# Performance work log

Measured on AMD Instinct MI355X. Metric: run time of the kernel, lower is better.

Reference implementation:

```python
import jax, jax.numpy as jnp
import numpy as np

B, TP, TF = 256, 128, 64
COV, D, OUT, CTRL, H, L = 64, 64, 32, 128, 512, 2


def _gru_layer(x, Wih, Whh, bih, bhh):
    # x: [B, T, in]; torch GRU gate order: r, z, n
    xg = jnp.einsum('bti,gi->btg', x, Wih) + bih  # [B, T, 3H]
    h0 = jnp.zeros((x.shape[0], Whh.shape[1]), x.dtype)

    def step(h, xg_t):
        gh = h @ Whh.T + bhh
        xr, xz, xn = jnp.split(xg_t, 3, axis=-1)
        hr, hz, hn = jnp.split(gh, 3, axis=-1)
        r = jax.nn.sigmoid(xr + hr)
        z = jax.nn.sigmoid(xz + hz)
        n = jnp.tanh(xn + r * hn)
        h = (1.0 - z) * n + z * h
        return h, h

    _, hs = jax.lax.scan(step, h0, jnp.swapaxes(xg, 0, 1))
    return jnp.swapaxes(hs, 0, 1)  # [B, T, H]


def setup_inputs() -> dict:
    key = jax.random.key(0)
    ks = jax.random.split(key, 32)
    s = 0.05
    inp = {
        'past_input': jax.random.normal(ks[0], (B, TP, COV), jnp.float32),
        'past_label': jax.random.normal(ks[1], (B, TP, OUT), jnp.float32),
        'future_input': jax.random.normal(ks[2], (B, TF, COV), jnp.float32),
        'gru_Wih_0': s * jax.random.normal(ks[3], (3 * H, COV), jnp.float32),
        'gru_Whh_0': s * jax.random.normal(ks[4], (3 * H, H), jnp.float32),
        'gru_bih_0': s * jax.random.normal(ks[5], (3 * H,), jnp.float32),
        'gru_bhh_0': s * jax.random.normal(ks[6], (3 * H,), jnp.float32),
        'gru_Wih_1': s * jax.random.normal(ks[7], (3 * H, H), jnp.float32),
        'gru_Whh_1': s * jax.random.normal(ks[8], (3 * H, H), jnp.float32),
        'gru_bih_1': s * jax.random.normal(ks[9], (3 * H,), jnp.float32),
        'gru_bhh_1': s * jax.random.normal(ks[10], (3 * H,), jnp.float32),
        'flow_u': s * jax.random.normal(ks[11], (D,), jnp.float32),
        'flow_w': s * jax.random.normal(ks[12], (D,), jnp.float32),
        'flow_b': s * jax.random.normal(ks[13], (D,), jnp.float32),
        'feat_W': s * jax.random.normal(ks[14], (D, H), jnp.float32),
        'feat_b': s * jax.random.normal(ks[15], (D,), jnp.float32),
        'ctrl_W1': s * jax.random.normal(ks[16], (CTRL, OUT), jnp.float32),
        'ctrl_b1': s * jax.random.normal(ks[17], (CTRL,), jnp.float32),
        'ctrl_W2': s * jax.random.normal(ks[18], (2 * D, CTRL), jnp.float32),
        'ctrl_b2': s * jax.random.normal(ks[19], (2 * D,), jnp.float32),
        'ctrlmu_W': s * jax.random.normal(ks[20], (D, D), jnp.float32),
        'ctrlmu_b': s * jax.random.normal(ks[21], (D,), jnp.float32),
        'out_W': s * jax.random.normal(ks[22], (OUT, D), jnp.float32),
        'out_b': s * jax.random.normal(ks[23], (OUT,), jnp.float32),
    }
    return inp


def reference(past_input, past_label, future_input,
              gru_Wih_0, gru_Whh_0, gru_bih_0, gru_bhh_0,
              gru_Wih_1, gru_Whh_1, gru_bih_1, gru_bhh_1,
              flow_u, flow_w, flow_b, feat_W, feat_b,
              ctrl_W1, ctrl_b1, ctrl_W2, ctrl_b2,
              ctrlmu_W, ctrlmu_b, out_W, out_b):
    cov = jnp.concatenate([past_input, future_input], axis=1)  # [B, T, COV]
    h1 = _gru_layer(cov, gru_Wih_0, gru_Whh_0, gru_bih_0, gru_bhh_0)
    cov_feat = _gru_layer(h1, gru_Wih_1, gru_Whh_1, gru_bih_1, gru_bhh_1)  # [B, T, H]
    Tp = past_input.shape[1]
    bsz = past_input.shape[0]

    def trans(mu_past, var_past, cov_t):
        # per-dim PlanarFlow vectorized over transition_dim
        a = jnp.tanh(flow_w * mu_past + flow_b)
        mu_prior = flow_u * a + cov_t @ feat_W.T + feat_b + mu_past
        coef = flow_u * flow_w * (1.0 - a * a)
        var_prior = 2.0 * coef * var_past + var_past + 1.0
        return mu_prior, var_prior

    def control(ctrl_in, mu_prior):
        hdn = jnp.tanh(ctrl_in @ ctrl_W1.T + ctrl_b1)
        cm, cls = jnp.split(hdn @ ctrl_W2.T + ctrl_b2, 2, axis=-1)
        cm = cm - (mu_prior @ ctrlmu_W.T + ctrlmu_b)
        return cm, jax.nn.softplus(cls)

    def fuse(mu_pr, var_pr, mu_po, var_po):
        s = var_po + var_pr
        mu_w = (var_po / s) * mu_pr + (var_pr / s) * mu_po
        return mu_w, var_pr * var_po / s

    def past_step(carry, xs):
        mu_post, var_post = carry
        cov_t, lab_t = xs
        mu_pr, var_pr = trans(mu_post, var_post, cov_t)
        pred = mu_pr @ out_W.T + out_b
        cm, cs = control(lab_t, mu_pr)
        return fuse(mu_pr, var_pr, cm, cs), (pred, cm, cs)

    def fut_step(carry, cov_t):
        mu_post, var_post = carry
        mu_pr, var_pr = trans(mu_post, var_post, cov_t)
        pred = mu_pr @ out_W.T + out_b
        cm, cs = control(pred, mu_pr)
        return fuse(mu_pr, var_pr, cm, cs), (pred, cm, cs)

    init = (jnp.zeros((bsz, D), cov.dtype), jnp.ones((bsz, D), cov.dtype))
    cov_p = jnp.swapaxes(cov_feat[:, :Tp], 0, 1)
    lab_p = jnp.swapaxes(past_label, 0, 1)
    carry, (pp, cmp_, csp) = jax.lax.scan(past_step, init, (cov_p, lab_p))
    cov_f = jnp.swapaxes(cov_feat[:, Tp:], 0, 1)
    _, (pf, cmf, csf) = jax.lax.scan(fut_step, carry, cov_f)

    pred = jnp.swapaxes(jnp.concatenate([pp, pf], axis=0), 0, 1)        # [B, T, OUT]
    cm = jnp.swapaxes(jnp.concatenate([cmp_, cmf], axis=0), 0, 1)[:, 1:]  # [B, T-1, D]
    cs = jnp.swapaxes(jnp.concatenate([csp, csf], axis=0), 0, 1)[:, 1:]   # [B, T-1, D]
    return pred, cm, cs
```

## Files before the change

kernel.cpp:

```cpp
#include <hip/hip_runtime.h>
#include <stdint.h>

#define DEV static __device__ __forceinline__

using short8 = __attribute__((ext_vector_type(8))) short;
using f32x4  = __attribute__((ext_vector_type(4))) float;
using gbl_u32 = const __attribute__((address_space(1))) unsigned int;
using lds_u32 = __attribute__((address_space(3))) unsigned int;

DEV float bf2f(short s) {
  unsigned u = ((unsigned)(unsigned short)s) << 16;
  float f; __builtin_memcpy(&f, &u, 4); return f;
}
DEV short f2bf(float f) {
  unsigned u; __builtin_memcpy(&u, &f, 4);
  u = (u + 0x7fffu + ((u >> 16) & 1u)) >> 16;
  return (short)u;
}
DEV void gload_lds16(const void* g, void* l) {
  __builtin_amdgcn_global_load_lds((gbl_u32*)g, (lds_u32*)l, 16, 0, 0);
}
DEV float sigm(float x) { return 1.f / (1.f + __expf(-x)); }
DEV float tanh_f(float x) {
  float e = __expf(2.f * x);
  return 1.f - 2.f * __builtin_amdgcn_rcpf(e + 1.f);
}
DEV unsigned load_sc0(const unsigned int* p) {
  unsigned v;
  asm volatile("global_load_dword %0, %1, off sc0\n\ts_waitcnt vmcnt(0)"
               : "=v"(v) : "v"(p) : "memory");
  return v;
}
DEV unsigned load_agent(const unsigned int* p) {
  return __hip_atomic_load(p, __ATOMIC_RELAXED, __HIP_MEMORY_SCOPE_AGENT);
}
DEV void bar() {
  asm volatile("s_waitcnt lgkmcnt(0)" ::: "memory");
  __builtin_amdgcn_sched_barrier(0);
  __builtin_amdgcn_s_barrier();
  __builtin_amdgcn_sched_barrier(0);
}

__global__ void pack_covf_k(const float* __restrict__ past, const float* __restrict__ fut,
                            short* __restrict__ covf) {
  const int n = 192 * 16 * 2 * 512;
  for (int i = blockIdx.x * blockDim.x + threadIdx.x; i < n; i += gridDim.x * blockDim.x) {
    int e = i & 7, l = (i >> 3) & 63, kf = (i >> 9) & 1, g = (i >> 10) & 15, t = i >> 14;
    int b = g * 16 + (l & 15);
    int col = kf * 32 + (l >> 4) * 8 + e;
    float v = (t < 128) ? past[((size_t)b * 128 + t) * 64 + col]
                        : fut[((size_t)b * 64 + (t - 128)) * 64 + col];
    covf[i] = f2bf(v);
  }
}

__global__ void pack_lab_k(const float* __restrict__ lab, short* __restrict__ labp) {
  const int n = 128 * 256 * 32;
  for (int i = blockIdx.x * blockDim.x + threadIdx.x; i < n; i += gridDim.x * blockDim.x) {
    int c = i & 31, r = i >> 5;
    int b = r & 255, t = r >> 8;
    labp[i] = f2bf(lab[((size_t)b * 128 + t) * 32 + c]);
  }
}

DEV int gru_srcrow(int pr) {
  int j = pr / 96, w = pr % 96;
  return ((w >> 5) << 9) + j * 32 + (w & 31);
}

__global__ void pack_gru_k(const float* __restrict__ Wih, const float* __restrict__ Whh,
                           const float* __restrict__ bih, const float* __restrict__ bhh,
                           int Kin, short* __restrict__ Wihp, short* __restrict__ Whhp,
                           float* __restrict__ bihp, float* __restrict__ bhhp) {
  const int nW1 = 1536 * Kin, nW2 = 1536 * 512;
  const int total = nW1 + nW2 + 3072;
  for (int idx = blockIdx.x * blockDim.x + threadIdx.x; idx < total; idx += gridDim.x * blockDim.x) {
    if (idx < nW1) {
      int pr = idx / Kin, k = idx - pr * Kin;
      Wihp[idx] = f2bf(Wih[(size_t)gru_srcrow(pr) * Kin + k]);
    } else if (idx < nW1 + nW2) {
      int ii = idx - nW1;
      int j = ii / 49152, r = ii - j * 49152;
      int i = r & 7, slot = r >> 3;
      int l = slot & 63, sf = slot >> 6;
      int kqg = sf / 6, tile = sf - kqg * 6;
      int w = tile * 16 + (l & 15);
      int k = kqg * 32 + (l >> 4) * 8 + i;
      int srow = (w >> 5) * 512 + j * 32 + (w & 31);
      Whhp[ii] = f2bf(Whh[(size_t)srow * 512 + k]);
    } else if (idx < nW1 + nW2 + 1536) {
      int pr = idx - nW1 - nW2;
      bihp[pr] = bih[gru_srcrow(pr)];
    } else {
      int pr = idx - nW1 - nW2 - 1536;
      bhhp[pr] = bhh[gru_srcrow(pr)];
    }
  }
}

__global__ void pack_wih0f_k(const float* __restrict__ Wih0, short* __restrict__ wf) {
  const int n = 16 * 6 * 2 * 512;
  for (int i = blockIdx.x * blockDim.x + threadIdx.x; i < n; i += gridDim.x * blockDim.x) {
    int j = i / 6144, r = i - j * 6144;
    int tile = r >> 10, kf = (r >> 9) & 1, l = (r >> 3) & 63, e = r & 7;
    int srow = gru_srcrow(j * 96 + tile * 16 + (l & 15));
    int k = kf * 32 + (l >> 4) * 8 + e;
    wf[i] = f2bf(Wih0[(size_t)srow * 64 + k]);
  }
}

__global__ void pack_misc_k(const float* __restrict__ fw, const float* __restrict__ w1,
                            const float* __restrict__ w2, short* __restrict__ fwb,
                            short* __restrict__ w1b, short* __restrict__ w2b) {
  const int n1 = 64 * 512, n2 = 128 * 32, n3 = 128 * 128;
  const int total = n1 + n2 + n3;
  for (int i = blockIdx.x * blockDim.x + threadIdx.x; i < total; i += gridDim.x * blockDim.x) {
    if (i < n1) fwb[i] = f2bf(fw[i]);
    else if (i < n1 + n2) w1b[i - n1] = f2bf(w1[i - n1]);
    else w2b[i - n1 - n2] = f2bf(w2[i - n1 - n2]);
  }
}

__global__ void pack_vae_k(const float* __restrict__ outW, const float* __restrict__ cmuW,
                           const float* __restrict__ W1, const float* __restrict__ W2,
                           short* __restrict__ vwf) {
  const int n = 52 * 512;
  for (int i = blockIdx.x * blockDim.x + threadIdx.x; i < n; i += gridDim.x * blockDim.x) {
    int fr = i >> 9, l = (i >> 3) & 63, e = i & 7;
    int lm = l & 15, lh = l >> 4;
    float v;
    if (fr < 4) { int kt = fr >> 1, nt = fr & 1; v = outW[(nt * 16 + lm) * 64 + kt * 32 + lh * 8 + e]; }
    else if (fr < 12) { int f = fr - 4, kt = f >> 2, nt = f & 3; v = cmuW[(nt * 16 + lm) * 64 + kt * 32 + lh * 8 + e]; }
    else if (fr < 20) { int nt = fr - 12; v = W1[(nt * 16 + lm) * 32 + lh * 8 + e]; }
    else { int f = fr - 20, kt = f >> 3, nt = f & 7; v = W2[(nt * 16 + lm) * 128 + kt * 32 + lh * 8 + e]; }
    vwf[i] = f2bf(v);
  }
}

template <int BK, bool OBF16, bool DOTANH, bool AFRAG, int CMODE = 0>
__global__ __launch_bounds__(256) void gemm_bt_k(
    const short* __restrict__ A, const short* __restrict__ Bw,
    const float* __restrict__ bias, void* __restrict__ Cout,
    int M, int N, int K) {
  constexpr int BM = 128, BN = 128;
  __shared__ short As[BM * BK];
  __shared__ short Bs[BN * BK];
  const int tid = threadIdx.x, lane = tid & 63;
  const int wave = tid >> 6, wm = wave >> 1, wn = wave & 1;
  const int bm = blockIdx.x, bn = blockIdx.y;
  const int lm = lane & 15, lk = (lane >> 4) * 8;
  f32x4 acc[4][4] = {};
  for (int k0 = 0; k0 < K; k0 += BK) {
    constexpr int BYTES = BM * BK * 2;
#pragma unroll
    for (int it = 0; it < BYTES / 4096; ++it) {
      int o = it * 4096 + tid * 16;
      if (AFRAG) {
        int sub = o >> 10, gl = sub >> 1, kk2 = sub & 1, inb = o & 1023;
        size_t region = ((size_t)(bm >> 1) * 16 + (bm & 1) * 8 + gl) * 16 + (k0 >> 5) + kk2;
        gload_lds16((const char*)A + region * 1024 + inb, (char*)As + (o - lane * 16));
      } else {
        int row = o / (BK * 2);
        int col = o - row * (BK * 2);
        const char* srcA = (const char*)A + (((size_t)(bm * BM + row)) * K + k0) * 2 + col;
        gload_lds16(srcA, (char*)As + (o - lane * 16));
      }
      int row = o / (BK * 2);
      int col = o - row * (BK * 2);
      int rb = bn * BN + row;
      if (rb >= N) rb = N - 1;
      const char* srcB = (const char*)Bw + (((size_t)rb) * K + k0) * 2 + col;
      gload_lds16(srcB, (char*)Bs + (o - lane * 16));
    }
    __syncthreads();
#pragma unroll
    for (int kk = 0; kk < BK / 32; ++kk) {
      short8 av[4], bv[4];
#pragma unroll
      for (int i = 0; i < 4; ++i) {
        if (AFRAG)
          av[i] = *(const short8*)((const char*)As + (((wm * 4 + i) * 2 + kk) << 10) + lane * 16);
        else
          av[i] = *(const short8*)((const char*)As + ((wm * 64 + i * 16 + lm) * BK + kk * 32 + lk) * 2);
      }
#pragma unroll
      for (int jv = 0; jv < 4; ++jv)
        bv[jv] = *(const short8*)((const char*)Bs + ((wn * 64 + jv * 16 + lm) * BK + kk * 32 + lk) * 2);
#pragma unroll
      for (int i = 0; i < 4; ++i)
#pragma unroll
        for (int jv = 0; jv < 4; ++jv)
          acc[i][jv] = __builtin_amdgcn_mfma_f32_16x16x32_bf16(av[i], bv[jv], acc[i][jv], 0, 0, 0);
    }
    __syncthreads();
  }
  if (CMODE == 1) {
    const int NT = N >> 4;
#pragma unroll
    for (int jv = 0; jv < 4; ++jv) {
      int col = bn * BN + wn * 64 + jv * 16 + lm;
      if (col >= N) continue;
      float bvl = bias[col];
#pragma unroll
      for (int i = 0; i < 4; ++i) {
        int rowblk = bm * 8 + wm * 4 + i;
        f32x4 v = acc[i][jv];
        v[0] += bvl; v[1] += bvl; v[2] += bvl; v[3] += bvl;
        *(f32x4*)((float*)Cout + (((size_t)rowblk * NT + (col >> 4)) << 8) + lane * 4) = v;
      }
    }
  } else {
#pragma unroll
    for (int jv = 0; jv < 4; ++jv) {
      int col = bn * BN + wn * 64 + jv * 16 + lm;
      if (col >= N) continue;
      float bvl = bias[col];
#pragma unroll
      for (int i = 0; i < 4; ++i) {
        int row0 = bm * BM + wm * 64 + i * 16 + (lane >> 4) * 4;
#pragma unroll
        for (int r = 0; r < 4; ++r) {
          float v = acc[i][jv][r] + bvl;
          if (DOTANH) v = tanhf(v);
          size_t off = (size_t)(row0 + r) * N + col;
          if (OBF16) ((short*)Cout)[off] = f2bf(v);
          else ((float*)Cout)[off] = v;
        }
      }
    }
  }
}

template <int SCHEME, int XGF>
__global__ __launch_bounds__(256) void gru_scan_k(
    const short* __restrict__ xg,
    const short* __restrict__ covf,
    const short* __restrict__ wihf_g,
    const short* __restrict__ Whhp,
    const float* __restrict__ bihp,
    const float* __restrict__ bhhp,
    short* __restrict__ hbuf,
    unsigned int* __restrict__ ctr,
    unsigned int* __restrict__ flags,
    int t0, int nsteps) {
  __shared__ short Wl[96 * 512];
  __shared__ short hs[16 * 512];
  __shared__ float sc[2][16 * 101];
  __shared__ float scx[2][16 * 33];
  __shared__ float bhs[96];
  __shared__ float bihn[32];
  const int tid = threadIdx.x, lane = tid & 63, wave = tid >> 6;
  const int x = blockIdx.x;
  const int g = (x & 7) + ((x >> 7) << 3);
  const int j = (x >> 3) & 15;
  unsigned int* __restrict__ myctr = ctr + g * 64;
  unsigned int* __restrict__ myflags = flags + g * 16;
  unsigned int* __restrict__ hbuf32 = (unsigned int*)hbuf;
  {
    const char* wsrc = (const char*)Whhp + (size_t)j * 98304;
#pragma unroll 4
    for (int it = 0; it < 24; ++it) {
      int o = it * 4096 + tid * 16;
      gload_lds16(wsrc + o, (char*)Wl + (o - lane * 16));
    }
    if (tid < 96) {
      float b = bhhp[j * 96 + tid];
      if (XGF && tid < 64) b += bihp[j * 96 + tid];
      bhs[tid] = b;
    }
    if (XGF && tid < 32) bihn[tid] = bihp[j * 96 + 64 + tid];
  }
  const int wk = wave >> 1, wn3 = wave & 1;
  const int m = tid >> 4, up = tid & 15, u0 = up * 2;
  short8 wihf0{}, wihf1{}, wihf2{};
  if (XGF) {
    wihf0 = *(const short8*)(wihf_g + ((size_t)(j * 6 + wn3 * 3 + 0) * 2 + wk) * 512 + lane * 8);
    wihf1 = *(const short8*)(wihf_g + ((size_t)(j * 6 + wn3 * 3 + 1) * 2 + wk) * 512 + lane * 8);
    wihf2 = *(const short8*)(wihf_g + ((size_t)(j * 6 + wn3 * 3 + 2) * 2 + wk) * 512 + lane * 8);
  }
  for (int tl = 0; tl < nsteps; ++tl) {
    const int t = t0 + tl;
    const char* hsrc = (const char*)hbuf + ((size_t)t * 16 + g) * 16384;
#pragma unroll
    for (int it = 0; it < 4; ++it) {
      int o = it * 4096 + tid * 16;
      gload_lds16(hsrc + o, (char*)hs + (o - lane * 16));
    }
    short8 cf{};
    unsigned int xr2 = 0, xz2 = 0, xn2 = 0;
    if (XGF) {
      cf = *(const short8*)(covf + (((size_t)t * 16 + g) * 2 + wk) * 512 + lane * 8);
    } else {
      const unsigned int* xp = (const unsigned int*)(xg + ((size_t)tl * 256 + g * 16 + m) * 1536 + j * 96);
      xr2 = xp[up]; xz2 = xp[16 + up]; xn2 = xp[32 + up];
    }
    __syncthreads();
    f32x4 a3[3] = {};
    f32x4 ax0 = {0.f, 0.f, 0.f, 0.f}, ax1 = {0.f, 0.f, 0.f, 0.f};
#pragma unroll
    for (int kq = 0; kq < 8; ++kq) {
      int kqg = wk * 8 + kq;
      short8 av = *(const short8*)((const char*)hs + (kqg << 10) + lane * 16);
#pragma unroll
      for (int n = 0; n < 3; ++n) {
        short8 bv = *(const short8*)((const char*)Wl + ((kqg * 6 + wn3 * 3 + n) << 10) + lane * 16);
        a3[n] = __builtin_amdgcn_mfma_f32_16x16x32_bf16(av, bv, a3[n], 0, 0, 0);
      }
    }
    if (XGF) {
      a3[0] = __builtin_amdgcn_mfma_f32_16x16x32_bf16(cf, wihf0, a3[0], 0, 0, 0);
      if (wn3 == 0) {
        a3[1] = __builtin_amdgcn_mfma_f32_16x16x32_bf16(cf, wihf1, a3[1], 0, 0, 0);
        a3[2] = __builtin_amdgcn_mfma_f32_16x16x32_bf16(cf, wihf2, a3[2], 0, 0, 0);
      } else {
        ax0 = __builtin_amdgcn_mfma_f32_16x16x32_bf16(cf, wihf1, ax0, 0, 0, 0);
        ax1 = __builtin_amdgcn_mfma_f32_16x16x32_bf16(cf, wihf2, ax1, 0, 0, 0);
      }
    }
#pragma unroll
    for (int n = 0; n < 3; ++n)
#pragma unroll
      for (int rr = 0; rr < 4; ++rr)
        sc[wk][((lane >> 4) * 4 + rr) * 101 + (wn3 * 3 + n) * 16 + (lane & 15)] = a3[n][rr];
    if (XGF && wn3 == 1) {
#pragma unroll
      for (int rr = 0; rr < 4; ++rr) {
        scx[wk][((lane >> 4) * 4 + rr) * 33 + (lane & 15)] = ax0[rr];
        scx[wk][((lane >> 4) * 4 + rr) * 33 + 16 + (lane & 15)] = ax1[rr];
      }
    }
    __syncthreads();
    {
      float Sr0 = sc[0][m * 101 + u0] + sc[1][m * 101 + u0];
      float Sr1 = sc[0][m * 101 + u0 + 1] + sc[1][m * 101 + u0 + 1];
      float Sz0 = sc[0][m * 101 + 32 + u0] + sc[1][m * 101 + 32 + u0];
      float Sz1 = sc[0][m * 101 + 33 + u0] + sc[1][m * 101 + 33 + u0];
      float Sn0 = sc[0][m * 101 + 64 + u0] + sc[1][m * 101 + 64 + u0];
      float Sn1 = sc[0][m * 101 + 65 + u0] + sc[1][m * 101 + 65 + u0];
      int hpa = ((j * 64 + (up >> 2) * 16 + m) << 4) + ((u0 & 7) << 1);
      unsigned int hpu = *(const unsigned int*)((const char*)hs + hpa);
      float hp0 = bf2f((short)(hpu & 0xffff)), hp1 = bf2f((short)(hpu >> 16));
      float r0, r1, z0, z1, n0, n1;
      if (XGF) {
        float Sx0 = scx[0][m * 33 + u0] + scx[1][m * 33 + u0];
        float Sx1 = scx[0][m * 33 + u0 + 1] + scx[1][m * 33 + u0 + 1];
        r0 = sigm(Sr0 + bhs[u0]);
        r1 = sigm(Sr1 + bhs[u0 + 1]);
        z0 = sigm(Sz0 + bhs[32 + u0]);
        z1 = sigm(Sz1 + bhs[33 + u0]);
        n0 = tanhf(Sx0 + bihn[u0] + r0 * (Sn0 + bhs[64 + u0]));
        n1 = tanhf(Sx1 + bihn[u0 + 1] + r1 * (Sn1 + bhs[65 + u0]));
      } else {
        r0 = sigm(bf2f((short)(xr2 & 0xffff)) + Sr0 + bhs[u0]);
        r1 = sigm(bf2f((short)(xr2 >> 16)) + Sr1 + bhs[u0 + 1]);
        z0 = sigm(bf2f((short)(xz2 & 0xffff)) + Sz0 + bhs[32 + u0]);
        z1 = sigm(bf2f((short)(xz2 >> 16)) + Sz1 + bhs[33 + u0]);
        n0 = tanhf(bf2f((short)(xn2 & 0xffff)) + r0 * (Sn0 + bhs[64 + u0]));
        n1 = tanhf(bf2f((short)(xn2 >> 16)) + r1 * (Sn1 + bhs[65 + u0]));
      }
      float h0 = (1.f - z0) * n0 + z0 * hp0;
      float h1 = (1.f - z1) * n1 + z1 * hp1;
      unsigned int hv = (unsigned int)(unsigned short)f2bf(h0) |
                        ((unsigned int)(unsigned short)f2bf(h1) << 16);
      size_t oi = ((size_t)(t + 1) * 16 + g) * 4096 +
                  (j * 64 + (up >> 2) * 16 + m) * 4 + (up & 3);
      __hip_atomic_store(hbuf32 + oi, hv, __ATOMIC_RELAXED, __HIP_MEMORY_SCOPE_AGENT);
    }
    __syncthreads();
    if constexpr (SCHEME == 1) {
      if (tid == 0) {
        __hip_atomic_fetch_add(myctr, 1u, __ATOMIC_RELAXED, __HIP_MEMORY_SCOPE_AGENT);
        const unsigned tgt = 16u * (unsigned)(tl + 1);
        int guard = 0;
        for (;;) {
          if (load_sc0(myctr) >= tgt) break;
          if (load_agent(myctr) >= tgt) break;
          if (++guard >= 200000) break;
        }
      }
    } else {
      const unsigned tgt = (unsigned)(tl + 1);
      if (tid == 0)
        __hip_atomic_store(myflags + j, tgt, __ATOMIC_RELAXED, __HIP_MEMORY_SCOPE_AGENT);
      if (tid < 16) {
        int guard = 0;
        for (;;) {
          if (load_sc0(myflags + tid) >= tgt) break;
          if (load_agent(myflags + tid) >= tgt) break;
          if (++guard >= 200000) break;
        }
      }
    }
    __syncthreads();
  }
}

#define PAST_STEP(T, FN, CMR, CSR)                                           \
  do {                                                                       \
    f32x4 muPr, varPr;                                                       \
    _Pragma("unroll") for (int r = 0; r < 4; ++r) {                          \
      float m_ = muC[r];                                                     \
      float a_ = tanh_f(fw1 * m_ + fb1);                                     \
      muPr[r] = fu1 * a_ + FN[r] + m_;                                       \
      float cf_ = fu1 * fw1 * (1.f - a_ * a_);                               \
      varPr[r] = 2.f * cf_ * varC[r] + varC[r] + 1.f;                        \
    }                                                                        \
    f32x4 cmNow = CMR, csNow = CSR;                                          \
    FN = *(const f32x4*)(feat_img + (((size_t)((T) + 2) * 16 + bg) * 4 + w) * 256 + l * 4); \
    if ((T) + 2 < 128) {                                                     \
      CMR = *(const f32x4*)(ctrl_img + (((size_t)((T) + 2) * 16 + bg) * 8 + w) * 256 + l * 4); \
      CSR = *(const f32x4*)(ctrl_img + (((size_t)((T) + 2) * 16 + bg) * 8 + 4 + w) * 256 + l * 4); \
    }                                                                        \
    _Pragma("unroll") for (int r = 0; r < 4; ++r) {                          \
      int row_ = m4 * 4 + r;                                                 \
      *(short*)((char*)muA + ((row_ * 128 + (w * 16 + c) * 2) ^ ((row_ & 7) << 4))) = f2bf(muPr[r]); \
    }                                                                        \
    bar();                                                                   \
    short8 muAf0 = *(const short8*)((const char*)muA + ((c * 128 + m4 * 16) ^ ((c & 7) << 4))); \
    short8 muAf1 = *(const short8*)((const char*)muA + ((c * 128 + 64 + m4 * 16) ^ ((c & 7) << 4))); \
    if (w == 0) *(short8*)(muprb + (((size_t)(T) * 16 + bg) * 2) * 512 + l * 8) = muAf0; \
    if (w == 1) *(short8*)(muprb + (((size_t)(T) * 16 + bg) * 2 + 1) * 512 + l * 8) = muAf1; \
    f32x4 mcC = {0.f, 0.f, 0.f, 0.f};                                        \
    mcC = __builtin_amdgcn_mfma_f32_16x16x32_bf16(muAf0, cmuf0, mcC, 0, 0, 0); \
    mcC = __builtin_amdgcn_mfma_f32_16x16x32_bf16(muAf1, cmuf1, mcC, 0, 0, 0); \
    bar();                                                                   \
    _Pragma("unroll") for (int r = 0; r < 4; ++r) {                          \
      float vp_ = varPr[r], mp_ = muPr[r];                                   \
      float cmv_ = cmNow[r] - (mcC[r] + cmub1);                              \
      float x_ = csNow[r];                                                   \
      float cs_ = (x_ > 20.f) ? x_ : __logf(1.f + __expf(x_));               \
      if ((T) >= 1) {                                                        \
        size_t b_ = (size_t)(bg * 16 + m4 * 4 + r);                          \
        out[1572864 + b_ * 12224 + (size_t)((T) - 1) * 64 + w * 16 + c] = cmv_; \
        out[4702208 + b_ * 12224 + (size_t)((T) - 1) * 64 + w * 16 + c] = cs_;  \
      }                                                                      \
      float s_ = cs_ + vp_;                                                  \
      float rs_ = __builtin_amdgcn_rcpf(s_);                                 \
      muC[r] = cs_ * rs_ * mp_ + vp_ * rs_ * cmv_;                           \
      varC[r] = vp_ * cs_ * rs_;                                             \
    }                                                                        \
  } while (0)

#define FUT_STEP(T, FN)                                                      \
  do {                                                                       \
    f32x4 muPr, varPr;                                                       \
    _Pragma("unroll") for (int r = 0; r < 4; ++r) {                          \
      float m_ = muC[r];                                                     \
      float a_ = tanh_f(fw1 * m_ + fb1);                                     \
      muPr[r] = fu1 * a_ + FN[r] + m_;                                       \
      float cf_ = fu1 * fw1 * (1.f - a_ * a_);                               \
      varPr[r] = 2.f * cf_ * varC[r] + varC[r] + 1.f;                        \
    }                                                                        \
    if ((T) + 2 < 192)                                                       \
      FN = *(const f32x4*)(feat_img + (((size_t)((T) + 2) * 16 + bg) * 4 + w) * 256 + l * 4); \
    _Pragma("unroll") for (int r = 0; r < 4; ++r) {                          \
      int row_ = m4 * 4 + r;                                                 \
      *(short*)((char*)muA + ((row_ * 128 + (w * 16 + c) * 2) ^ ((row_ & 7) << 4))) = f2bf(muPr[r]); \
    }                                                                        \
    bar();                                                                   \
    short8 muAf0 = *(const short8*)((const char*)muA + ((c * 128 + m4 * 16) ^ ((c & 7) << 4))); \
    short8 muAf1 = *(const short8*)((const char*)muA + ((c * 128 + 64 + m4 * 16) ^ ((c & 7) << 4))); \
    f32x4 mcC = {0.f, 0.f, 0.f, 0.f};                                        \
    mcC = __builtin_amdgcn_mfma_f32_16x16x32_bf16(muAf0, cmuf0, mcC, 0, 0, 0); \
    mcC = __builtin_amdgcn_mfma_f32_16x16x32_bf16(muAf1, cmuf1, mcC, 0, 0, 0); \
    if (w < 2) {                                                             \
      f32x4 predC = {0.f, 0.f, 0.f, 0.f};                                    \
      predC = __builtin_amdgcn_mfma_f32_16x16x32_bf16(muAf0, outWf0, predC, 0, 0, 0); \
      predC = __builtin_amdgcn_mfma_f32_16x16x32_bf16(muAf1, outWf1, predC, 0, 0, 0); \
      _Pragma("unroll") for (int r = 0; r < 4; ++r) {                        \
        float pv_ = predC[r] + outb1;                                        \
        out[(size_t)(bg * 16 + m4 * 4 + r) * 6144 + (T) * 32 + w * 16 + c] = pv_; \
        int row_ = m4 * 4 + r;                                               \
        *(short*)((char*)predA + ((row_ * 64 + (w * 16 + c) * 2) ^ ((row_ & 3) << 4))) = f2bf(pv_); \
      }                                                                      \
    }                                                                        \
    bar();                                                                   \
    short8 pAf = *(const short8*)((const char*)predA + ((c * 64 + m4 * 16) ^ ((c & 3) << 4))); \
    f32x4 z0 = {0.f, 0.f, 0.f, 0.f}, z1 = {0.f, 0.f, 0.f, 0.f};              \
    z0 = __builtin_amdgcn_mfma_f32_16x16x32_bf16(pAf, *(const short8*)((const char*)Wctl + (2 * w) * 1024 + l * 16), z0, 0, 0, 0); \
    z1 = __builtin_amdgcn_mfma_f32_16x16x32_bf16(pAf, *(const short8*)((const char*)Wctl + (2 * w + 1) * 1024 + l * 16), z1, 0, 0, 0); \
    _Pragma("unroll") for (int r = 0; r < 4; ++r) {                          \
      int row_ = m4 * 4 + r;                                                 \
      *(short*)((char*)hdnA + ((row_ * 256 + ((2 * w) * 16 + c) * 2) ^ ((row_ & 7) << 4))) = f2bf(tanh_f(z0[r] + b1a)); \
      *(short*)((char*)hdnA + ((row_ * 256 + ((2 * w + 1) * 16 + c) * 2) ^ ((row_ & 7) << 4))) = f2bf(tanh_f(z1[r] + b1b)); \
    }                                                                        \
    bar();                                                                   \
    short8 hAf0 = *(const short8*)((const char*)hdnA + ((c * 256 + 0 * 64 + m4 * 16) ^ ((c & 7) << 4))); \
    short8 hAf1 = *(const short8*)((const char*)hdnA + ((c * 256 + 1 * 64 + m4 * 16) ^ ((c & 7) << 4))); \
    short8 hAf2 = *(const short8*)((const char*)hdnA + ((c * 256 + 2 * 64 + m4 * 16) ^ ((c & 7) << 4))); \
    short8 hAf3 = *(const short8*)((const char*)hdnA + ((c * 256 + 3 * 64 + m4 * 16) ^ ((c & 7) << 4))); \
    f32x4 zcm = {0.f, 0.f, 0.f, 0.f}, zcs = {0.f, 0.f, 0.f, 0.f};            \
    zcm = __builtin_amdgcn_mfma_f32_16x16x32_bf16(hAf0, *(const short8*)((const char*)Wctl + (8 + 0 * 8 + w) * 1024 + l * 16), zcm, 0, 0, 0); \
    zcm = __builtin_amdgcn_mfma_f32_16x16x32_bf16(hAf1, *(const short8*)((const char*)Wctl + (8 + 1 * 8 + w) * 1024 + l * 16), zcm, 0, 0, 0); \
    zcm = __builtin_amdgcn_mfma_f32_16x16x32_bf16(hAf2, *(const short8*)((const char*)Wctl + (8 + 2 * 8 + w) * 1024 + l * 16), zcm, 0, 0, 0); \
    zcm = __builtin_amdgcn_mfma_f32_16x16x32_bf16(hAf3, *(const short8*)((const char*)Wctl + (8 + 3 * 8 + w) * 1024 + l * 16), zcm, 0, 0, 0); \
    zcs = __builtin_amdgcn_mfma_f32_16x16x32_bf16(hAf0, *(const short8*)((const char*)Wctl + (8 + 0 * 8 + 4 + w) * 1024 + l * 16), zcs, 0, 0, 0); \
    zcs = __builtin_amdgcn_mfma_f32_16x16x32_bf16(hAf1, *(const short8*)((const char*)Wctl + (8 + 1 * 8 + 4 + w) * 1024 + l * 16), zcs, 0, 0, 0); \
    zcs = __builtin_amdgcn_mfma_f32_16x16x32_bf16(hAf2, *(const short8*)((const char*)Wctl + (8 + 2 * 8 + 4 + w) * 1024 + l * 16), zcs, 0, 0, 0); \
    zcs = __builtin_amdgcn_mfma_f32_16x16x32_bf16(hAf3, *(const short8*)((const char*)Wctl + (8 + 3 * 8 + 4 + w) * 1024 + l * 16), zcs, 0, 0, 0); \
    bar();                                                                   \
    _Pragma("unroll") for (int r = 0; r < 4; ++r) {                          \
      float vp_ = varPr[r], mp_ = muPr[r];                                   \
      float cmv_ = (zcm[r] + b2cm) - (mcC[r] + cmub1);                       \
      float x_ = zcs[r] + b2cs;                                              \
      float cs_ = (x_ > 20.f) ? x_ : __logf(1.f + __expf(x_));               \
      size_t b_ = (size_t)(bg * 16 + m4 * 4 + r);                            \
      out[1572864 + b_ * 12224 + (size_t)((T) - 1) * 64 + w * 16 + c] = cmv_; \
      out[4702208 + b_ * 12224 + (size_t)((T) - 1) * 64 + w * 16 + c] = cs_;  \
      float s_ = cs_ + vp_;                                                  \
      float rs_ = __builtin_amdgcn_rcpf(s_);                                 \
      muC[r] = cs_ * rs_ * mp_ + vp_ * rs_ * cmv_;                           \
      varC[r] = vp_ * cs_ * rs_;                                             \
    }                                                                        \
  } while (0)

__global__ __launch_bounds__(256) void vae_k(
    const float* __restrict__ feat_img, const float* __restrict__ ctrl_img,
    const short* __restrict__ vwf,
    const float* __restrict__ flow_u, const float* __restrict__ flow_w,
    const float* __restrict__ flow_b, const float* __restrict__ outb,
    const float* __restrict__ b1, const float* __restrict__ b2,
    const float* __restrict__ cmub, short* __restrict__ muprb,
    float* __restrict__ out) {
  __shared__ short Wctl[40 * 512];
  __shared__ short muA[16 * 64];
  __shared__ short predA[16 * 32];
  __shared__ short hdnA[16 * 128];
  const int tid = threadIdx.x, l = tid & 63, w = tid >> 6;
  const int m4 = l >> 4, c = l & 15, bg = blockIdx.x;
  {
    const char* src = (const char*)vwf + 12288;
#pragma unroll
    for (int it = 0; it < 10; ++it) {
      int o = it * 4096 + tid * 16;
      gload_lds16(src + o, (char*)Wctl + (o - l * 16));
    }
  }
  short8 cmuf0 = *(const short8*)(vwf + (4 + w) * 512 + l * 8);
  short8 cmuf1 = *(const short8*)(vwf + (8 + w) * 512 + l * 8);
  short8 outWf0 = *(const short8*)(vwf + ((w & 1)) * 512 + l * 8);
  short8 outWf1 = *(const short8*)(vwf + (2 + (w & 1)) * 512 + l * 8);
  float fw1 = flow_w[w * 16 + c], fu1 = flow_u[w * 16 + c];
  float fb1 = flow_b[w * 16 + c], cmub1 = cmub[w * 16 + c];
  float outb1 = outb[(w & 1) * 16 + c];
  float b1a = b1[(2 * w) * 16 + c], b1b = b1[(2 * w + 1) * 16 + c];
  float b2cm = b2[w * 16 + c], b2cs = b2[(4 + w) * 16 + c];
  f32x4 muC = {0.f, 0.f, 0.f, 0.f}, varC = {1.f, 1.f, 1.f, 1.f};
  f32x4 fN0 = *(const f32x4*)(feat_img + ((size_t)bg * 4 + w) * 256 + l * 4);
  f32x4 fN1 = *(const f32x4*)(feat_img + ((size_t)(16 + bg) * 4 + w) * 256 + l * 4);
  f32x4 cmA = *(const f32x4*)(ctrl_img + ((size_t)bg * 8 + w) * 256 + l * 4);
  f32x4 csA = *(const f32x4*)(ctrl_img + ((size_t)bg * 8 + 4 + w) * 256 + l * 4);
  f32x4 cmB = *(const f32x4*)(ctrl_img + ((size_t)(16 + bg) * 8 + w) * 256 + l * 4);
  f32x4 csB = *(const f32x4*)(ctrl_img + ((size_t)(16 + bg) * 8 + 4 + w) * 256 + l * 4);
  __syncthreads();
  for (int t2 = 0; t2 < 128; t2 += 2) {
    PAST_STEP(t2, fN0, cmA, csA);
    PAST_STEP(t2 + 1, fN1, cmB, csB);
  }
  asm volatile("s_waitcnt vmcnt(0)" ::: "memory");
  __builtin_amdgcn_sched_barrier(0);
  __builtin_amdgcn_s_barrier();
  for (int t2 = 128; t2 < 192; t2 += 2) {
    FUT_STEP(t2, fN0);
    FUT_STEP(t2 + 1, fN1);
  }
}

__global__ __launch_bounds__(512) void pred_past_k(
    const short* __restrict__ muprb, const short* __restrict__ vwf,
    const float* __restrict__ outb, float* __restrict__ out) {
  const int l = threadIdx.x & 63;
  const int w = blockIdx.x * 8 + (threadIdx.x >> 6);
  const int t = w >> 4, bg = w & 15;
  const int m4 = l >> 4, c = l & 15;
  short8 a0 = *(const short8*)(muprb + ((size_t)w * 2 + 0) * 512 + l * 8);
  short8 a1 = *(const short8*)(muprb + ((size_t)w * 2 + 1) * 512 + l * 8);
  float outb2[2] = {outb[c], outb[16 + c]};
#pragma unroll
  for (int nt = 0; nt < 2; ++nt) {
    short8 w0 = *(const short8*)(vwf + (0 * 2 + nt) * 512 + l * 8);
    short8 w1 = *(const short8*)(vwf + (1 * 2 + nt) * 512 + l * 8);
    f32x4 p = {0.f, 0.f, 0.f, 0.f};
    p = __builtin_amdgcn_mfma_f32_16x16x32_bf16(a0, w0, p, 0, 0, 0);
    p = __builtin_amdgcn_mfma_f32_16x16x32_bf16(a1, w1, p, 0, 0, 0);
#pragma unroll
    for (int r = 0; r < 4; ++r)
      out[(size_t)(bg * 16 + m4 * 4 + r) * 6144 + t * 32 + nt * 16 + c] = p[r] + outb2[nt];
  }
}

extern "C" void kernel_launch(void* const* d_in, const int* in_sizes, int n_in,
                              void* d_out, int out_size, void* d_ws, size_t ws_size,
                              hipStream_t stream) {
  (void)in_sizes; (void)n_in; (void)out_size; (void)ws_size;
  const float* past_input = (const float*)d_in[0];
  const float* past_label = (const float*)d_in[1];
  const float* future_input = (const float*)d_in[2];
  const float* Wih0 = (const float*)d_in[3];
  const float* Whh0 = (const float*)d_in[4];
  const float* bih0 = (const float*)d_in[5];
  const float* bhh0 = (const float*)d_in[6];
  const float* Wih1 = (const float*)d_in[7];
  const float* Whh1 = (const float*)d_in[8];
  const float* bih1 = (const float*)d_in[9];
  const float* bhh1 = (const float*)d_in[10];
  const float* flow_u = (const float*)d_in[11];
  const float* flow_w = (const float*)d_in[12];
  const float* flow_b = (const float*)d_in[13];
  const float* feat_W = (const float*)d_in[14];
  const float* feat_b = (const float*)d_in[15];
  const float* ctrl_W1 = (const float*)d_in[16];
  const float* ctrl_b1 = (const float*)d_in[17];
  const float* ctrl_W2 = (const float*)d_in[18];
  const float* ctrl_b2 = (const float*)d_in[19];
  const float* cmuW = (const float*)d_in[20];
  const float* cmub = (const float*)d_in[21];
  const float* outW = (const float*)d_in[22];
  const float* outb = (const float*)d_in[23];

  char* ws = (char*)d_ws;
  size_t off = 0;
  auto alloc = [&](size_t bytes) -> char* {
    char* p = ws + off;
    off += (bytes + 255) & ~(size_t)255;
    return p;
  };
  short* covf  = (short*)alloc(192ull * 16 * 2 * 512 * 2);
  short* labp  = (short*)alloc(32768ull * 32 * 2);
  short* Wih0p = (short*)alloc(1536ull * 64 * 2);
  short* Whh0p = (short*)alloc(1536ull * 512 * 2);
  short* Wih1p = (short*)alloc(1536ull * 512 * 2);
  short* Whh1p = (short*)alloc(1536ull * 512 * 2);
  float* bih0p = (float*)alloc(1536 * 4);
  float* bhh0p = (float*)alloc(1536 * 4);
  float* bih1p = (float*)alloc(1536 * 4);
  float* bhh1p = (float*)alloc(1536 * 4);
  short* featWb = (short*)alloc(64ull * 512 * 2);
  short* W1b   = (short*)alloc(128ull * 32 * 2);
  short* W2b   = (short*)alloc(128ull * 128 * 2);
  short* vwf   = (short*)alloc(52ull * 512 * 2);
  short* wih0f = (short*)alloc(16ull * 6 * 2 * 512 * 2);
  short* xgc   = (short*)alloc(48ull * 256 * 1536 * 2);
  short* h1buf = (short*)alloc(193ull * 256 * 512 * 2);
  short* cfbuf = (short*)alloc(193ull * 256 * 512 * 2);
  unsigned int* ctr = (unsigned int*)alloc(8 * 16 * 64 * 4);
  unsigned int* flg = (unsigned int*)alloc(8 * 16 * 16 * 4);
  float* feat_img = (float*)xgc;
  short* hdnb     = (short*)((char*)xgc + 12582912);
  float* ctrl_img = (float*)((char*)xgc + 20971520);
  short* muprb    = (short*)covf;

  hipMemsetAsync(ctr, 0, 8 * 16 * 64 * 4, stream);
  hipMemsetAsync(flg, 0, 8 * 16 * 16 * 4, stream);
  hipMemsetAsync(h1buf, 0, 256 * 512 * 2, stream);
  hipMemsetAsync(cfbuf, 0, 256 * 512 * 2, stream);

  pack_covf_k<<<2048, 256, 0, stream>>>(past_input, future_input, covf);
  pack_lab_k<<<1024, 256, 0, stream>>>(past_label, labp);
  pack_gru_k<<<1024, 256, 0, stream>>>(Wih0, Whh0, bih0, bhh0, 64, Wih0p, Whh0p, bih0p, bhh0p);
  pack_gru_k<<<1024, 256, 0, stream>>>(Wih1, Whh1, bih1, bhh1, 512, Wih1p, Whh1p, bih1p, bhh1p);
  pack_wih0f_k<<<96, 256, 0, stream>>>(Wih0, wih0f);
  pack_misc_k<<<64, 256, 0, stream>>>(feat_W, ctrl_W1, ctrl_W2, featWb, W1b, W2b);
  pack_vae_k<<<104, 256, 0, stream>>>(outW, cmuW, ctrl_W1, ctrl_W2, vwf);

  gru_scan_k<2, 1><<<256, 256, 0, stream>>>(
      nullptr, covf, wih0f, Whh0p, bih0p, bhh0p, h1buf,
      ctr, flg, 0, 192);
  for (int c = 0; c < 4; ++c) {
    gemm_bt_k<64, true, false, true><<<dim3(96, 12), 256, 0, stream>>>(
        h1buf + (size_t)(1 + c * 48) * 131072, Wih1p, bih1p, xgc, 12288, 1536, 512);
    int d = 4 + c;
    if (c & 1)
      gru_scan_k<2, 0><<<256, 256, 0, stream>>>(
          xgc, nullptr, nullptr, Whh1p, nullptr, bhh1p, cfbuf,
          ctr + d * 1024, flg + d * 256, c * 48, 48);
    else
      gru_scan_k<1, 0><<<256, 256, 0, stream>>>(
          xgc, nullptr, nullptr, Whh1p, nullptr, bhh1p, cfbuf,
          ctr + d * 1024, flg + d * 256, c * 48, 48);
  }
  gemm_bt_k<64, false, false, true, 1><<<dim3(384, 1), 256, 0, stream>>>(
      cfbuf + 131072, featWb, feat_b, feat_img, 49152, 64, 512);
  gemm_bt_k<32, true, true, false><<<dim3(256, 1), 256, 0, stream>>>(
      labp, W1b, ctrl_b1, hdnb, 32768, 128, 32);
  gemm_bt_k<64, false, false, false, 1><<<dim3(256, 1), 256, 0, stream>>>(
      hdnb, W2b, ctrl_b2, ctrl_img, 32768, 128, 128);

  vae_k<<<16, 256, 0, stream>>>(feat_img, ctrl_img, vwf, flow_u, flow_w, flow_b,
                                outb, ctrl_b1, ctrl_b2, cmub, muprb, (float*)d_out);
  pred_past_k<<<256, 512, 0, stream>>>(muprb, vwf, outb, (float*)d_out);
}
```

Baseline: 1.349 ms.

## Interleave two batch groups per GRU scan block to hide barrier latency

The GRU scan kernels now launch 128 blocks instead of 256. Each block owns one weight slice and alternates between two batch groups (gA, gB), with double-buffered h and score LDS. The cross-block wait moves to the start of each step, so waiting on one group's flags overlaps with computing the other group. The counter-based SCHEME 1 barrier is dropped and only per-slice flags remain. In the layer-0 kernel, the extra n-gate input-projection MFMAs are concentrated in one wave and the scx reduction is removed. This halves grid parallelism and keeps the spin-wait guard, which risks serialising work if the overlap does not materialise.

```diff
diff --git a/kernel.cpp b/kernel.cpp
--- a/kernel.cpp
+++ b/kernel.cpp
@@ -231,8 +231,8 @@
   }
 }
 
-template <int SCHEME, int XGF>
-__global__ __launch_bounds__(256) void gru_scan_k(
+template <int XGF>
+__global__ __launch_bounds__(256) void gru2_scan_k(
     const short* __restrict__ xg,
     const short* __restrict__ covf,
     const short* __restrict__ wihf_g,
@@ -240,21 +240,19 @@
     const float* __restrict__ bihp,
     const float* __restrict__ bhhp,
     short* __restrict__ hbuf,
-    unsigned int* __restrict__ ctr,
     unsigned int* __restrict__ flags,
     int t0, int nsteps) {
   __shared__ short Wl[96 * 512];
-  __shared__ short hs[16 * 512];
-  __shared__ float sc[2][16 * 101];
+  __shared__ short hs[2][16 * 512];
+  __shared__ float sc[2][2][16 * 97];
   __shared__ float scx[2][16 * 33];
   __shared__ float bhs[96];
   __shared__ float bihn[32];
   const int tid = threadIdx.x, lane = tid & 63, wave = tid >> 6;
   const int x = blockIdx.x;
-  const int g = (x & 7) + ((x >> 7) << 3);
+  const int s = x & 7;
   const int j = (x >> 3) & 15;
-  unsigned int* __restrict__ myctr = ctr + g * 64;
-  unsigned int* __restrict__ myflags = flags + g * 16;
+  const int gA = s, gB = s + 8;
   unsigned int* __restrict__ hbuf32 = (unsigned int*)hbuf;
   {
     const char* wsrc = (const char*)Whhp + (size_t)j * 98304;
@@ -272,24 +270,45 @@
   }
   const int wk = wave >> 1, wn3 = wave & 1;
   const int m = tid >> 4, up = tid & 15, u0 = up * 2;
-  short8 wihf0{}, wihf1{}, wihf2{};
+  short8 wihf0{}, wihf1{}, wihf2{}, wn4a{}, wn4b{}, wn5a{}, wn5b{};
   if (XGF) {
-    wihf0 = *(const short8*)(wihf_g + ((size_t)(j * 6 + wn3 * 3 + 0) * 2 + wk) * 512 + lane * 8);
-    wihf1 = *(const short8*)(wihf_g + ((size_t)(j * 6 + wn3 * 3 + 1) * 2 + wk) * 512 + lane * 8);
-    wihf2 = *(const short8*)(wihf_g + ((size_t)(j * 6 + wn3 * 3 + 2) * 2 + wk) * 512 + lane * 8);
-  }
-  for (int tl = 0; tl < nsteps; ++tl) {
+    auto FR = [&](int tile, int kf) {
+      return *(const short8*)(wihf_g + ((size_t)(j * 6 + tile) * 2 + kf) * 512 + lane * 8);
+    };
+    if (wn3 == 0) {
+      wihf0 = FR(0, wk); wihf1 = FR(1, wk); wihf2 = FR(2, wk);
+    } else {
+      wihf0 = FR(3, wk);
+      if (wk == 0) { wn4a = FR(4, 0); wn4b = FR(4, 1); wn5a = FR(5, 0); wn5b = FR(5, 1); }
+    }
+  }
+  auto STEP = [&](int g, int gi, int tl) {
     const int t = t0 + tl;
+    if (tl > 0) {
+      const unsigned tgt = (unsigned)tl;
+      if (tid < 16) {
+        const unsigned int* fp = flags + g * 16 + tid;
+        int guard = 0;
+        for (;;) {
+          if (load_sc0(fp) >= tgt) break;
+          if (load_agent(fp) >= tgt) break;
+          if (++guard >= 200000) break;
+        }
+      }
+    }
+    __syncthreads();
     const char* hsrc = (const char*)hbuf + ((size_t)t * 16 + g) * 16384;
 #pragma unroll
     for (int it = 0; it < 4; ++it) {
       int o = it * 4096 + tid * 16;
-      gload_lds16(hsrc + o, (char*)hs + (o - lane * 16));
-    }
-    short8 cf{};
+      gload_lds16(hsrc + o, (char*)hs[gi] + (o - lane * 16));
+    }
+    short8 cf0{}, cf1{};
     unsigned int xr2 = 0, xz2 = 0, xn2 = 0;
     if (XGF) {
-      cf = *(const short8*)(covf + (((size_t)t * 16 + g) * 2 + wk) * 512 + lane * 8);
+      cf0 = *(const short8*)(covf + (((size_t)t * 16 + g) * 2 + wk) * 512 + lane * 8);
+      if (wn3 == 1 && wk == 0)
+        cf1 = *(const short8*)(covf + (((size_t)t * 16 + g) * 2 + 1) * 512 + lane * 8);
     } else {
       const unsigned int* xp = (const unsigned int*)(xg + ((size_t)tl * 256 + g * 16 + m) * 1536 + j * 96);
       xr2 = xp[up]; xz2 = xp[16 + up]; xn2 = xp[32 + up];
@@ -300,7 +319,7 @@
 #pragma unroll
     for (int kq = 0; kq < 8; ++kq) {
       int kqg = wk * 8 + kq;
-      short8 av = *(const short8*)((const char*)hs + (kqg << 10) + lane * 16);
+      short8 av = *(const short8*)((const char*)hs[gi] + (kqg << 10) + lane * 16);
 #pragma unroll
       for (int n = 0; n < 3; ++n) {
         short8 bv = *(const short8*)((const char*)Wl + ((kqg * 6 + wn3 * 3 + n) << 10) + lane * 16);
@@ -308,42 +327,44 @@
       }
     }
     if (XGF) {
-      a3[0] = __builtin_amdgcn_mfma_f32_16x16x32_bf16(cf, wihf0, a3[0], 0, 0, 0);
+      a3[0] = __builtin_amdgcn_mfma_f32_16x16x32_bf16(cf0, wihf0, a3[0], 0, 0, 0);
       if (wn3 == 0) {
-        a3[1] = __builtin_amdgcn_mfma_f32_16x16x32_bf16(cf, wihf1, a3[1], 0, 0, 0);
-        a3[2] = __builtin_amdgcn_mfma_f32_16x16x32_bf16(cf, wihf2, a3[2], 0, 0, 0);
-      } else {
-        ax0 = __builtin_amdgcn_mfma_f32_16x16x32_bf16(cf, wihf1, ax0, 0, 0, 0);
-        ax1 = __builtin_amdgcn_mfma_f32_16x16x32_bf16(cf, wihf2, ax1, 0, 0, 0);
+        a3[1] = __builtin_amdgcn_mfma_f32_16x16x32_bf16(cf0, wihf1, a3[1], 0, 0, 0);
+        a3[2] = __builtin_amdgcn_mfma_f32_16x16x32_bf16(cf0, wihf2, a3[2], 0, 0, 0);
+      } else if (wk == 0) {
+        ax0 = __builtin_amdgcn_mfma_f32_16x16x32_bf16(cf0, wn4a, ax0, 0, 0, 0);
+        ax0 = __builtin_amdgcn_mfma_f32_16x16x32_bf16(cf1, wn4b, ax0, 0, 0, 0);
+        ax1 = __builtin_amdgcn_mfma_f32_16x16x32_bf16(cf0, wn5a, ax1, 0, 0, 0);
+        ax1 = __builtin_amdgcn_mfma_f32_16x16x32_bf16(cf1, wn5b, ax1, 0, 0, 0);
       }
     }
 #pragma unroll
     for (int n = 0; n < 3; ++n)
 #pragma unroll
       for (int rr = 0; rr < 4; ++rr)
-        sc[wk][((lane >> 4) * 4 + rr) * 101 + (wn3 * 3 + n) * 16 + (lane & 15)] = a3[n][rr];
-    if (XGF && wn3 == 1) {
+        sc[gi][wk][((lane >> 4) * 4 + rr) * 97 + (wn3 * 3 + n) * 16 + (lane & 15)] = a3[n][rr];
+    if (XGF && wn3 == 1 && wk == 0) {
 #pragma unroll
       for (int rr = 0; rr < 4; ++rr) {
-        scx[wk][((lane >> 4) * 4 + rr) * 33 + (lane & 15)] = ax0[rr];
-        scx[wk][((lane >> 4) * 4 + rr) * 33 + 16 + (lane & 15)] = ax1[rr];
+        scx[gi][((lane >> 4) * 4 + rr) * 33 + (lane & 15)] = ax0[rr];
+        scx[gi][((lane >> 4) * 4 + rr) * 33 + 16 + (lane & 15)] = ax1[rr];
       }
     }
     __syncthreads();
     {
-      float Sr0 = sc[0][m * 101 + u0] + sc[1][m * 101 + u0];
-      float Sr1 = sc[0][m * 101 + u0 + 1] + sc[1][m * 101 + u0 + 1];
-      float Sz0 = sc[0][m * 101 + 32 + u0] + sc[1][m * 101 + 32 + u0];
-      float Sz1 = sc[0][m * 101 + 33 + u0] + sc[1][m * 101 + 33 + u0];
-      float Sn0 = sc[0][m * 101 + 64 + u0] + sc[1][m * 101 + 64 + u0];
-      float Sn1 = sc[0][m * 101 + 65 + u0] + sc[1][m * 101 + 65 + u0];
+      float Sr0 = sc[gi][0][m * 97 + u0] + sc[gi][1][m * 97 + u0];
+      float Sr1 = sc[gi][0][m * 97 + u0 + 1] + sc[gi][1][m * 97 + u0 + 1];
+      float Sz0 = sc[gi][0][m * 97 + 32 + u0] + sc[gi][1][m * 97 + 32 + u0];
+      float Sz1 = sc[gi][0][m * 97 + 33 + u0] + sc[gi][1][m * 97 + 33 + u0];
+      float Sn0 = sc[gi][0][m * 97 + 64 + u0] + sc[gi][1][m * 97 + 64 + u0];
+      float Sn1 = sc[gi][0][m * 97 + 65 + u0] + sc[gi][1][m * 97 + 65 + u0];
       int hpa = ((j * 64 + (up >> 2) * 16 + m) << 4) + ((u0 & 7) << 1);
-      unsigned int hpu = *(const unsigned int*)((const char*)hs + hpa);
+      unsigned int hpu = *(const unsigned int*)((const char*)hs[gi] + hpa);
       float hp0 = bf2f((short)(hpu & 0xffff)), hp1 = bf2f((short)(hpu >> 16));
       float r0, r1, z0, z1, n0, n1;
       if (XGF) {
-        float Sx0 = scx[0][m * 33 + u0] + scx[1][m * 33 + u0];
-        float Sx1 = scx[0][m * 33 + u0 + 1] + scx[1][m * 33 + u0 + 1];
+        float Sx0 = scx[gi][m * 33 + u0];
+        float Sx1 = scx[gi][m * 33 + u0 + 1];
         r0 = sigm(Sr0 + bhs[u0]);
         r1 = sigm(Sr1 + bhs[u0 + 1]);
         z0 = sigm(Sz0 + bhs[32 + u0]);
@@ -367,31 +388,13 @@
       __hip_atomic_store(hbuf32 + oi, hv, __ATOMIC_RELAXED, __HIP_MEMORY_SCOPE_AGENT);
     }
     __syncthreads();
-    if constexpr (SCHEME == 1) {
-      if (tid == 0) {
-        __hip_atomic_fetch_add(myctr, 1u, __ATOMIC_RELAXED, __HIP_MEMORY_SCOPE_AGENT);
-        const unsigned tgt = 16u * (unsigned)(tl + 1);
-        int guard = 0;
-        for (;;) {
-          if (load_sc0(myctr) >= tgt) break;
-          if (load_agent(myctr) >= tgt) break;
-          if (++guard >= 200000) break;
-        }
-      }
-    } else {
-      const unsigned tgt = (unsigned)(tl + 1);
-      if (tid == 0)
-        __hip_atomic_store(myflags + j, tgt, __ATOMIC_RELAXED, __HIP_MEMORY_SCOPE_AGENT);
-      if (tid < 16) {
-        int guard = 0;
-        for (;;) {
-          if (load_sc0(myflags + tid) >= tgt) break;
-          if (load_agent(myflags + tid) >= tgt) break;
-          if (++guard >= 200000) break;
-        }
-      }
-    }
-    __syncthreads();
+    if (tid == 0)
+      __hip_atomic_store(flags + g * 16 + j, (unsigned)(tl + 1),
+                         __ATOMIC_RELAXED, __HIP_MEMORY_SCOPE_AGENT);
+  };
+  for (int tl = 0; tl < nsteps; ++tl) {
+    STEP(gA, 0, tl);
+    STEP(gB, 1, tl);
   }
 }
 
@@ -643,14 +646,12 @@
   short* xgc   = (short*)alloc(48ull * 256 * 1536 * 2);
   short* h1buf = (short*)alloc(193ull * 256 * 512 * 2);
   short* cfbuf = (short*)alloc(193ull * 256 * 512 * 2);
-  unsigned int* ctr = (unsigned int*)alloc(8 * 16 * 64 * 4);
   unsigned int* flg = (unsigned int*)alloc(8 * 16 * 16 * 4);
   float* feat_img = (float*)xgc;
   short* hdnb     = (short*)((char*)xgc + 12582912);
   float* ctrl_img = (float*)((char*)xgc + 20971520);
   short* muprb    = (short*)covf;
 
-  hipMemsetAsync(ctr, 0, 8 * 16 * 64 * 4, stream);
   hipMemsetAsync(flg, 0, 8 * 16 * 16 * 4, stream);
   hipMemsetAsync(h1buf, 0, 256 * 512 * 2, stream);
   hipMemsetAsync(cfbuf, 0, 256 * 512 * 2, stream);
@@ -663,21 +664,14 @@
   pack_misc_k<<<64, 256, 0, stream>>>(feat_W, ctrl_W1, ctrl_W2, featWb, W1b, W2b);
   pack_vae_k<<<104, 256, 0, stream>>>(outW, cmuW, ctrl_W1, ctrl_W2, vwf);
 
-  gru_scan_k<2, 1><<<256, 256, 0, stream>>>(
-      nullptr, covf, wih0f, Whh0p, bih0p, bhh0p, h1buf,
-      ctr, flg, 0, 192);
+  gru2_scan_k<1><<<128, 256, 0, stream>>>(
+      nullptr, covf, wih0f, Whh0p, bih0p, bhh0p, h1buf, flg, 0, 192);
   for (int c = 0; c < 4; ++c) {
     gemm_bt_k<64, true, false, true><<<dim3(96, 12), 256, 0, stream>>>(
         h1buf + (size_t)(1 + c * 48) * 131072, Wih1p, bih1p, xgc, 12288, 1536, 512);
-    int d = 4 + c;
-    if (c & 1)
-      gru_scan_k<2, 0><<<256, 256, 0, stream>>>(
-          xgc, nullptr, nullptr, Whh1p, nullptr, bhh1p, cfbuf,
-          ctr + d * 1024, flg + d * 256, c * 48, 48);
-    else
-      gru_scan_k<1, 0><<<256, 256, 0, stream>>>(
-          xgc, nullptr, nullptr, Whh1p, nullptr, bhh1p, cfbuf,
-          ctr + d * 1024, flg + d * 256, c * 48, 48);
+    gru2_scan_k<0><<<128, 256, 0, stream>>>(
+        xgc, nullptr, nullptr, Whh1p, nullptr, bhh1p, cfbuf,
+        flg + (1 + c) * 256, c * 48, 48);
   }
   gemm_bt_k<64, false, false, true, 1><<<dim3(384, 1), 256, 0, stream>>>(
       cfbuf + 131072, featWb, feat_b, feat_img, 49152, 64, 512);
```

New measurement: 1.981 ms. +46.9%, slower.

## Defer GRU step barrier wait to start of next step, unify flag scheme

Applied to the files above, without the earlier changes.

The per-step cross-block synchronisation in the GRU scan now signals completion at the end of a step and waits on the 16 peer flags at the start of the next step. This removes the trailing wait after the last step. The counter-based scheme and the sc0 polling loads are dropped, so every scan launch uses per-block flags polled with agent-scope atomic loads. The design depends on relaxed atomic stores and loads for visibility of h across blocks, and the spin guard is now 400000 iterations.

```diff
diff --git a/kernel.cpp b/kernel.cpp
--- a/kernel.cpp
+++ b/kernel.cpp
@@ -24,12 +24,6 @@
 DEV float tanh_f(float x) {
   float e = __expf(2.f * x);
   return 1.f - 2.f * __builtin_amdgcn_rcpf(e + 1.f);
-}
-DEV unsigned load_sc0(const unsigned int* p) {
-  unsigned v;
-  asm volatile("global_load_dword %0, %1, off sc0\n\ts_waitcnt vmcnt(0)"
-               : "=v"(v) : "v"(p) : "memory");
-  return v;
 }
 DEV unsigned load_agent(const unsigned int* p) {
   return __hip_atomic_load(p, __ATOMIC_RELAXED, __HIP_MEMORY_SCOPE_AGENT);
@@ -231,7 +225,7 @@
   }
 }
 
-template <int SCHEME, int XGF>
+template <int XGF>
 __global__ __launch_bounds__(256) void gru_scan_k(
     const short* __restrict__ xg,
     const short* __restrict__ covf,
@@ -240,7 +234,6 @@
     const float* __restrict__ bihp,
     const float* __restrict__ bhhp,
     short* __restrict__ hbuf,
-    unsigned int* __restrict__ ctr,
     unsigned int* __restrict__ flags,
     int t0, int nsteps) {
   __shared__ short Wl[96 * 512];
@@ -253,7 +246,6 @@
   const int x = blockIdx.x;
   const int g = (x & 7) + ((x >> 7) << 3);
   const int j = (x >> 3) & 15;
-  unsigned int* __restrict__ myctr = ctr + g * 64;
   unsigned int* __restrict__ myflags = flags + g * 16;
   unsigned int* __restrict__ hbuf32 = (unsigned int*)hbuf;
   {
@@ -280,6 +272,15 @@
   }
   for (int tl = 0; tl < nsteps; ++tl) {
     const int t = t0 + tl;
+    if (tl > 0) {
+      const unsigned tgt = (unsigned)tl;
+      if (tid < 16) {
+        const unsigned int* fp = myflags + tid;
+        int guard = 0;
+        while (load_agent(fp) < tgt && ++guard < 400000) {}
+      }
+    }
+    __syncthreads();
     const char* hsrc = (const char*)hbuf + ((size_t)t * 16 + g) * 16384;
 #pragma unroll
     for (int it = 0; it < 4; ++it) {
@@ -367,30 +368,9 @@
       __hip_atomic_store(hbuf32 + oi, hv, __ATOMIC_RELAXED, __HIP_MEMORY_SCOPE_AGENT);
     }
     __syncthreads();
-    if constexpr (SCHEME == 1) {
-      if (tid == 0) {
-        __hip_atomic_fetch_add(myctr, 1u, __ATOMIC_RELAXED, __HIP_MEMORY_SCOPE_AGENT);
-        const unsigned tgt = 16u * (unsigned)(tl + 1);
-        int guard = 0;
-        for (;;) {
-          if (load_sc0(myctr) >= tgt) break;
-          if (load_agent(myctr) >= tgt) break;
-          if (++guard >= 200000) break;
-        }
-      }
-    } else {
-      const unsigned tgt = (unsigned)(tl + 1);
-      if (tid == 0)
-        __hip_atomic_store(myflags + j, tgt, __ATOMIC_RELAXED, __HIP_MEMORY_SCOPE_AGENT);
-      if (tid < 16) {
-        int guard = 0;
-        for (;;) {
-          if (load_sc0(myflags + tid) >= tgt) break;
-          if (load_agent(myflags + tid) >= tgt) break;
-          if (++guard >= 200000) break;
-        }
-      }
-    }
+    if (tid == 0)
+      __hip_atomic_store(myflags + j, (unsigned)(tl + 1),
+                         __ATOMIC_RELAXED, __HIP_MEMORY_SCOPE_AGENT);
     __syncthreads();
   }
 }
@@ -643,14 +623,12 @@
   short* xgc   = (short*)alloc(48ull * 256 * 1536 * 2);
   short* h1buf = (short*)alloc(193ull * 256 * 512 * 2);
   short* cfbuf = (short*)alloc(193ull * 256 * 512 * 2);
-  unsigned int* ctr = (unsigned int*)alloc(8 * 16 * 64 * 4);
   unsigned int* flg = (unsigned int*)alloc(8 * 16 * 16 * 4);
   float* feat_img = (float*)xgc;
   short* hdnb     = (short*)((char*)xgc + 12582912);
   float* ctrl_img = (float*)((char*)xgc + 20971520);
   short* muprb    = (short*)covf;
 
-  hipMemsetAsync(ctr, 0, 8 * 16 * 64 * 4, stream);
   hipMemsetAsync(flg, 0, 8 * 16 * 16 * 4, stream);
   hipMemsetAsync(h1buf, 0, 256 * 512 * 2, stream);
   hipMemsetAsync(cfbuf, 0, 256 * 512 * 2, stream);
@@ -663,21 +641,14 @@
   pack_misc_k<<<64, 256, 0, stream>>>(feat_W, ctrl_W1, ctrl_W2, featWb, W1b, W2b);
   pack_vae_k<<<104, 256, 0, stream>>>(outW, cmuW, ctrl_W1, ctrl_W2, vwf);
 
-  gru_scan_k<2, 1><<<256, 256, 0, stream>>>(
-      nullptr, covf, wih0f, Whh0p, bih0p, bhh0p, h1buf,
-      ctr, flg, 0, 192);
+  gru_scan_k<1><<<256, 256, 0, stream>>>(
+      nullptr, covf, wih0f, Whh0p, bih0p, bhh0p, h1buf, flg, 0, 192);
   for (int c = 0; c < 4; ++c) {
     gemm_bt_k<64, true, false, true><<<dim3(96, 12), 256, 0, stream>>>(
         h1buf + (size_t)(1 + c * 48) * 131072, Wih1p, bih1p, xgc, 12288, 1536, 512);
-    int d = 4 + c;
-    if (c & 1)
-      gru_scan_k<2, 0><<<256, 256, 0, stream>>>(
-          xgc, nullptr, nullptr, Whh1p, nullptr, bhh1p, cfbuf,
-          ctr + d * 1024, flg + d * 256, c * 48, 48);
-    else
-      gru_scan_k<1, 0><<<256, 256, 0, stream>>>(
-          xgc, nullptr, nullptr, Whh1p, nullptr, bhh1p, cfbuf,
-          ctr + d * 1024, flg + d * 256, c * 48, 48);
+    gru_scan_k<0><<<256, 256, 0, stream>>>(
+        xgc, nullptr, nullptr, Whh1p, nullptr, bhh1p, cfbuf,
+        flg + (1 + c) * 256, c * 48, 48);
   }
   gemm_bt_k<64, false, false, true, 1><<<dim3(384, 1), 256, 0, stream>>>(
       cfbuf + 131072, featWb, feat_b, feat_img, 49152, 64, 512);
```

Measured after the change: 1.369 ms. Within noise of the previous version (+1.5%).
